# Kernel tuning notes

Measured on AMD Instinct MI355X. Metric: run time of the kernel, lower is better.

The kernel has to match this reference:

```python
import jax, jax.numpy as jnp
import numpy as np

B, S, E, H = 4, 2048, 1024, 16
HD = E // H  # 64


def setup_inputs() -> dict:
    key = jax.random.key(0)
    k1, k2, k3, k4, k5 = jax.random.split(key, 5)
    scale = 0.02
    return {
        "hidden_states": jax.random.normal(k1, (B, S, E), dtype=jnp.float32),
        "c_attn_w": jax.random.normal(k2, (E, 3 * E), dtype=jnp.float32) * scale,
        "c_attn_b": jnp.zeros((3 * E,), dtype=jnp.float32),
        "c_proj_w": jax.random.normal(k3, (E, E), dtype=jnp.float32) * scale,
        "c_proj_b": jnp.zeros((E,), dtype=jnp.float32),
    }


def reference(hidden_states, c_attn_w, c_attn_b, c_proj_w, c_proj_b):
    b, s, e = hidden_states.shape
    h, hd = H, HD
    # Conv1D: x @ W + b
    qkv = hidden_states @ c_attn_w + c_attn_b                     # [B,S,3E]
    # Faithful to source: split heads BEFORE splitting q/k/v
    qkv = qkv.reshape(b, s, h, 3 * hd).transpose(0, 2, 1, 3)      # [B,H,S,3*hd]
    q, k, v = jnp.split(qkv, 3, axis=-1)                          # each [B,H,S,hd]
    scores = jnp.einsum("bhqd,bhkd->bhqk", q, k) / (hd ** 0.5)    # [B,H,S,S]
    causal = jnp.tril(jnp.ones((s, s), dtype=bool))
    masked_bias = jnp.asarray(-10000.0, dtype=scores.dtype)
    scores = jnp.where(causal, scores, masked_bias)
    attn_weights = jax.nn.softmax(scores, axis=-1)                # [B,H,S,S]
    attn_out = jnp.einsum("bhqk,bhkd->bhqd", attn_weights, v)     # [B,H,S,hd]
    attn_out = attn_out.transpose(0, 2, 1, 3).reshape(b, s, e)    # merge heads
    out = attn_out @ c_proj_w + c_proj_b                          # [B,S,E]
    return out
```

## Files before the change

### kernel.cpp

```cpp
#include <hip/hip_runtime.h>

typedef __attribute__((ext_vector_type(8))) __bf16 bf16x8;
typedef __attribute__((ext_vector_type(2))) __bf16 bf16x2;
typedef __attribute__((ext_vector_type(8))) unsigned short u16x8;
typedef __attribute__((ext_vector_type(4))) float f32x4;
typedef __attribute__((ext_vector_type(16))) float f32x16;
typedef __attribute__((ext_vector_type(2))) unsigned int u32x2;
typedef __attribute__((ext_vector_type(4))) unsigned int u32x4;
typedef unsigned short u16;
typedef unsigned int u32;

constexpr int Bb = 4, Ss = 2048, Ee = 1024, Hh = 16, HDd = 64;
constexpr int Mm = Bb * Ss;
constexpr int N3 = 3 * Ee;
constexpr float QSC = 0.18033688011112042f;
constexpr int BHSTRIDE = Ss * HDd;
constexpr float M0 = 8.0f;

__device__ __forceinline__ u16 f2bf(float f) {
  u32 u = __builtin_bit_cast(u32, f);
  u = (u + 0x7FFFu + ((u >> 16) & 1u)) >> 16;
  return (u16)u;
}
__device__ __forceinline__ u32 pk2(float a, float b) {
  bf16x2 t;
  t[0] = (__bf16)a;
  t[1] = (__bf16)b;
  return __builtin_bit_cast(u32, t);
}
__device__ __forceinline__ float ex2(float x) {
#if __has_builtin(__builtin_amdgcn_exp2f)
  return __builtin_amdgcn_exp2f(x);
#else
  float r;
  asm volatile("v_exp_f32 %0, %1" : "=v"(r) : "v"(x));
  return r;
#endif
}

__device__ __forceinline__ void gload_lds16(const void* g, void* l) {
  __builtin_amdgcn_global_load_lds(
      (__attribute__((address_space(1))) void*)g,
      (__attribute__((address_space(3))) void*)l, 16, 0, 0);
}

__device__ __forceinline__ f32x4 mfma16(bf16x8 a, bf16x8 b, f32x4 c) {
  return __builtin_amdgcn_mfma_f32_16x16x32_bf16(a, b, c, 0, 0, 0);
}
__device__ __forceinline__ f32x16 mfma32(bf16x8 a, bf16x8 b, f32x16 c) {
  return __builtin_amdgcn_mfma_f32_32x32x16_bf16(a, b, c, 0, 0, 0);
}

__global__ void cast_x_kernel(const float* __restrict__ x, u16* __restrict__ xb, int n4) {
  int i = blockIdx.x * blockDim.x + threadIdx.x;
  int stride = gridDim.x * blockDim.x;
  for (; i < n4; i += stride) {
    float4 v = reinterpret_cast<const float4*>(x)[i];
    ushort4 o;
    o.x = f2bf(v.x); o.y = f2bf(v.y); o.z = f2bf(v.z); o.w = f2bf(v.w);
    reinterpret_cast<ushort4*>(xb)[i] = o;
  }
}

__global__ void transpose_cast_kernel(const float* __restrict__ W, u16* __restrict__ Wt,
                                      int K, int N) {
  __shared__ float tile[32][33];
  int n0 = blockIdx.x * 32, k0 = blockIdx.y * 32;
  int tx = threadIdx.x & 31, ty = threadIdx.x >> 5;
#pragma unroll
  for (int i = 0; i < 4; ++i)
    tile[ty + i * 8][tx] = W[(size_t)(k0 + ty + i * 8) * N + n0 + tx];
  __syncthreads();
#pragma unroll
  for (int i = 0; i < 4; ++i)
    Wt[(size_t)(n0 + ty + i * 8) * K + k0 + tx] = f2bf(tile[tx][ty + i * 8]);
}

template <int MODE>
__global__ __launch_bounds__(512, 1) void gemm_pipe(
    const u16* __restrict__ A, const u16* __restrict__ Bt,
    const float* __restrict__ bias, int xtiles, int cpx,
    float* __restrict__ Cout, u16* __restrict__ Qr,
    u16* __restrict__ Kp, u16* __restrict__ Vp) {
  extern __shared__ __attribute__((aligned(16))) u16 dyn[];
  constexpr int K = 1024, NT = 16;
  constexpr int BUFSTRIDE = 24576;

  int f = blockIdx.x;
  int swz = (f & 7) * cpx + (f >> 3);
  int bx = swz % xtiles, by = swz / xtiles;
  int m0 = by * 128, n0 = bx * 256;

  int tid = threadIdx.x, lane = tid & 63, wid = tid >> 6;
  int wr = wid >> 2, wc = wid & 3;
  int l7 = lane & 7, l8 = lane >> 3;
  int swcol = (l7 ^ l8) * 8;

  const u16* Ab = A + (size_t)(m0 + l8) * K + swcol;
  const u16* Bb = Bt + (size_t)(n0 + l8) * K + swcol;

  f32x4 acc[4][4];
  const f32x4 fz = {0.f, 0.f, 0.f, 0.f};
#pragma unroll
  for (int mi = 0; mi < 4; ++mi)
#pragma unroll
    for (int nj = 0; nj < 4; ++nj) acc[mi][nj] = fz;

  auto STA = [&](int tt, int c) {
    int ch = wid * 2 + c;
    gload_lds16(Ab + (size_t)(ch * 8) * K + tt * 64,
                dyn + (tt % 3) * BUFSTRIDE + ch * 512);
  };
  auto STB = [&](int tt, int c) {
    int ch = wid * 4 + c;
    gload_lds16(Bb + (size_t)(ch * 8) * K + tt * 64,
                dyn + (tt % 3) * BUFSTRIDE + 8192 + ch * 512);
  };
  auto LDA = [&](const u16* buf, int mi, int ks) -> bf16x8 {
    int row = wr * 64 + mi * 16 + (lane & 15);
    int j = ((ks * 4 + (lane >> 4)) ^ l7) * 8;
    return *(const bf16x8*)&buf[row * 64 + j];
  };
  auto LDB = [&](const u16* buf, int ni, int ks) -> bf16x8 {
    int row = wc * 64 + ni * 16 + (lane & 15);
    int j = ((ks * 4 + (lane >> 4)) ^ l7) * 8;
    return *(const bf16x8*)&buf[row * 64 + j];
  };

#pragma unroll
  for (int c = 0; c < 2; ++c) STA(0, c);
#pragma unroll
  for (int c = 0; c < 4; ++c) STB(0, c);
#pragma unroll
  for (int c = 0; c < 2; ++c) STA(1, c);
#pragma unroll
  for (int c = 0; c < 4; ++c) STB(1, c);

  for (int t = 0; t < NT; ++t) {
    const u16* Ar = dyn + (t % 3) * BUFSTRIDE;
    const u16* Br = Ar + 8192;
    if (t + 1 < NT)
      asm volatile("s_waitcnt vmcnt(6)" ::: "memory");
    else
      asm volatile("s_waitcnt vmcnt(0)" ::: "memory");
    __builtin_amdgcn_sched_barrier(0);
    __builtin_amdgcn_s_barrier();
    __builtin_amdgcn_sched_barrier(0);

    bool pre2 = (t + 2) < NT;
#pragma unroll
    for (int kk = 0; kk < 2; ++kk) {
      bf16x8 af[4], bfr[4];
#pragma unroll
      for (int mi = 0; mi < 4; ++mi) af[mi] = LDA(Ar, mi, kk);
#pragma unroll
      for (int ni = 0; ni < 4; ++ni) bfr[ni] = LDB(Br, ni, kk);
      if (kk == 0 && pre2) { STA(t + 2, 0); STA(t + 2, 1); }
      if (kk == 1 && pre2) { STB(t + 2, 0); STB(t + 2, 1); STB(t + 2, 2); STB(t + 2, 3); }
      __builtin_amdgcn_s_setprio(1);
#pragma unroll
      for (int mi = 0; mi < 4; ++mi)
#pragma unroll
        for (int ni = 0; ni < 4; ++ni)
          acc[mi][ni] = mfma16(af[mi], bfr[ni], acc[mi][ni]);
      __builtin_amdgcn_s_setprio(0);
      asm volatile("" ::: "memory");
    }
  }
  __syncthreads();

  if (MODE == 0) {
    int Nn = xtiles * 256;
#pragma unroll
    for (int nj = 0; nj < 4; ++nj) {
      int n = n0 + wc * 64 + nj * 16 + (lane & 15);
      float bn = bias[n];
#pragma unroll
      for (int mi = 0; mi < 4; ++mi)
#pragma unroll
        for (int r = 0; r < 4; ++r) {
          int m = m0 + wr * 64 + mi * 16 + (lane >> 4) * 4 + r;
          Cout[(size_t)m * Nn + n] = acc[mi][nj][r] + bn;
        }
    }
  } else {
    int gi0 = bx * 4;
    int bb = m0 >> 11;
    int mrow0 = m0 & 2047;
#pragma unroll
    for (int p = 0; p < 2; ++p) {
      if ((wc >> 1) == p) {
        int gg = wc & 1;
        int gi = gi0 + p * 2 + gg;
        int typ = gi % 3;
        float cs = (typ == 0) ? QSC : 1.0f;
#pragma unroll
        for (int nj = 0; nj < 4; ++nj) {
          int dl = nj * 16 + (lane & 15);
          float bn = bias[gi * 64 + dl];
#pragma unroll
          for (int mi = 0; mi < 4; ++mi)
#pragma unroll
            for (int r = 0; r < 4; ++r) {
              int row = wr * 64 + mi * 16 + (lane >> 4) * 4 + r;
              dyn[(gg * 128 + row) * 72 + dl] = f2bf((acc[mi][nj][r] + bn) * cs);
            }
        }
      }
      __syncthreads();
#pragma unroll
      for (int gg = 0; gg < 2; ++gg) {
        int gi = gi0 + p * 2 + gg;
        int typ = gi % 3, h = gi / 3;
        size_t basebh = (size_t)(bb * 16 + h) * BHSTRIDE;
        if (typ == 2) {
#pragma unroll
          for (int i = 0; i < 2; ++i) {
            int c = tid + 512 * i;
            int dl = c & 63, s64 = (c >> 6) & 1, kv8 = c >> 7;
            u16x8 val;
            int lrow = gg * 128 + s64 * 64 + kv8 * 8;
#pragma unroll
            for (int e = 0; e < 8; ++e) val[e] = dyn[(lrow + e) * 72 + dl];
            int tile = (mrow0 >> 6) + s64;
            size_t o = basebh + (size_t)tile * 4096 + (dl >> 5) * 2048 +
                       (kv8 >> 1) * 512 + (kv8 & 1) * 256 + (dl & 31) * 8;
            *(u16x8*)(Vp + o) = val;
          }
        } else {
#pragma unroll
          for (int i = 0; i < 2; ++i) {
            int c = tid + 512 * i;
            int sl = c >> 3, dc = c & 7;
            u16x8 val = *(const u16x8*)&dyn[(gg * 128 + sl) * 72 + dc * 8];
            int srw = mrow0 + sl;
            if (typ == 0) {
              *(u16x8*)(Qr + basebh + (size_t)srw * 64 + dc * 8) = val;
            } else {
              int tile = srw >> 6, rl = srw & 63;
              size_t o = basebh + (size_t)tile * 4096 + (rl >> 5) * 2048 +
                         (dc >> 1) * 512 + (dc & 1) * 256 + (rl & 31) * 8;
              *(u16x8*)(Kp + o) = val;
            }
          }
        }
      }
      __syncthreads();
    }
  }
}

__global__ __launch_bounds__(256) void attn_kernel(const u16* __restrict__ Qr,
                                                   const u16* __restrict__ Kp,
                                                   const u16* __restrict__ Vp,
                                                   u16* __restrict__ aout) {
  __shared__ float mbuf[2][64][33];

  int bh = blockIdx.x;
  int j = gridDim.y - 1 - blockIdx.y;
  int tid = threadIdx.x, w = tid >> 6, lane = tid & 63;
  int hi = lane >> 5, ln31 = lane & 31;
  int qrow = 32 * j + ln31;
  int nt = (j >> 1) + 1;
  int par = (j & 1) ? 32 : 0;

  size_t basebh = (size_t)bh * BHSTRIDE;
  const u16* kpb = Kp + basebh + hi * 256 + ln31 * 8;
  const u16* vpb = Vp + basebh + hi * 256 + ln31 * 8;

  bf16x8 qf[4];
#pragma unroll
  for (int kc = 0; kc < 4; ++kc)
    qf[kc] = *(const bf16x8*)(Qr + basebh + (size_t)qrow * 64 + kc * 16 + hi * 8);

  f32x16 o[2];
#pragma unroll
  for (int dm = 0; dm < 2; ++dm)
#pragma unroll
    for (int e = 0; e < 16; ++e) o[dm][e] = 0.f;
  float lrun = 0.f;

  for (int t = w; t < nt; t += 4) {
    const u16* kpt = kpb + (size_t)t * 4096;
    const u16* vpt = vpb + (size_t)t * 4096;
    bf16x8 kf[2][4], vf[2][4];
#pragma unroll
    for (int mt = 0; mt < 2; ++mt)
#pragma unroll
      for (int kc = 0; kc < 4; ++kc)
        kf[mt][kc] = *(const bf16x8*)(kpt + mt * 2048 + kc * 512);
#pragma unroll
    for (int dm = 0; dm < 2; ++dm)
#pragma unroll
      for (int kw = 0; kw < 4; ++kw)
        vf[dm][kw] = *(const bf16x8*)(vpt + dm * 2048 + kw * 512);

    f32x16 sc[2];
#pragma unroll
    for (int mt = 0; mt < 2; ++mt)
#pragma unroll
      for (int e = 0; e < 16; ++e) sc[mt][e] = -M0;
    __builtin_amdgcn_s_setprio(1);
#pragma unroll
    for (int mt = 0; mt < 2; ++mt)
#pragma unroll
      for (int kc = 0; kc < 4; ++kc)
        sc[mt] = mfma32(kf[mt][kc], qf[kc], sc[mt]);
    __builtin_amdgcn_s_setprio(0);

    if (t == nt - 1) {
#pragma unroll
      for (int mt = 0; mt < 2; ++mt)
#pragma unroll
        for (int r = 0; r < 16; ++r) {
          bool msk = (32 * mt + (r & 3) + 8 * (r >> 2) + 4 * hi) > (ln31 + par);
          sc[mt][r] = msk ? -__builtin_inff() : sc[mt][r];
        }
    }
    float s0a = 0.f, s1a = 0.f, s2a = 0.f, s3a = 0.f;
#pragma unroll
    for (int mt = 0; mt < 2; ++mt)
#pragma unroll
      for (int r = 0; r < 16; ++r) {
        float e = ex2(sc[mt][r]);
        sc[mt][r] = e;
        if ((r & 3) == 0) s0a += e;
        else if ((r & 3) == 1) s1a += e;
        else if ((r & 3) == 2) s2a += e;
        else s3a += e;
      }
    float sum = (s0a + s1a) + (s2a + s3a);
    sum += __shfl_xor(sum, 32);
    lrun += sum;

#pragma unroll
    for (int kw = 0; kw < 4; ++kw) {
      int mt = kw >> 1, k8 = (kw & 1) * 8;
      u32 a0 = pk2(sc[mt][k8 + 0], sc[mt][k8 + 1]);
      u32 a1 = pk2(sc[mt][k8 + 2], sc[mt][k8 + 3]);
      u32 b0 = pk2(sc[mt][k8 + 4], sc[mt][k8 + 5]);
      u32 b1 = pk2(sc[mt][k8 + 6], sc[mt][k8 + 7]);
      u32x2 r0 = __builtin_amdgcn_permlane32_swap(a0, b0, false, false);
      u32x2 r1 = __builtin_amdgcn_permlane32_swap(a1, b1, false, false);
      u32x4 fw;
      fw.x = r0.x;
      fw.y = r1.x;
      fw.z = r0.y;
      fw.w = r1.y;
      bf16x8 pf = __builtin_bit_cast(bf16x8, fw);
      __builtin_amdgcn_s_setprio(1);
#pragma unroll
      for (int dm = 0; dm < 2; ++dm)
        o[dm] = mfma32(vf[dm][kw], pf, o[dm]);
      __builtin_amdgcn_s_setprio(0);
    }
  }

  if (w >= 2) {
    mbuf[w - 2][lane][0] = lrun;
#pragma unroll
    for (int dm = 0; dm < 2; ++dm)
#pragma unroll
      for (int e = 0; e < 16; ++e) mbuf[w - 2][lane][1 + dm * 16 + e] = o[dm][e];
  }
  __syncthreads();
  if (w < 2) {
    lrun += mbuf[w][lane][0];
#pragma unroll
    for (int dm = 0; dm < 2; ++dm)
#pragma unroll
      for (int e = 0; e < 16; ++e) o[dm][e] += mbuf[w][lane][1 + dm * 16 + e];
  }
  __syncthreads();
  if (w == 1) {
    mbuf[0][lane][0] = lrun;
#pragma unroll
    for (int dm = 0; dm < 2; ++dm)
#pragma unroll
      for (int e = 0; e < 16; ++e) mbuf[0][lane][1 + dm * 16 + e] = o[dm][e];
  }
  __syncthreads();
  if (w == 0) {
    lrun += mbuf[0][lane][0];
#pragma unroll
    for (int dm = 0; dm < 2; ++dm)
#pragma unroll
      for (int e = 0; e < 16; ++e) o[dm][e] += mbuf[0][lane][1 + dm * 16 + e];
    int b = bh >> 4, h = bh & 15;
    float inv = 1.f / lrun;
    u16* orow = aout + (size_t)(b * Ss + qrow) * Ee + h * HDd;
#pragma unroll
    for (int dm = 0; dm < 2; ++dm)
#pragma unroll
      for (int g = 0; g < 4; ++g) {
        ushort4 st;
        st.x = f2bf(o[dm][4 * g + 0] * inv);
        st.y = f2bf(o[dm][4 * g + 1] * inv);
        st.z = f2bf(o[dm][4 * g + 2] * inv);
        st.w = f2bf(o[dm][4 * g + 3] * inv);
        *(ushort4*)(orow + 32 * dm + 8 * g + 4 * hi) = st;
      }
  }
}

extern "C" void kernel_launch(void* const* d_in, const int* in_sizes, int n_in,
                              void* d_out, int out_size, void* d_ws, size_t ws_size,
                              hipStream_t stream) {
  const float* hs        = (const float*)d_in[0];
  const float* c_attn_w  = (const float*)d_in[1];
  const float* c_attn_b  = (const float*)d_in[2];
  const float* c_proj_w  = (const float*)d_in[3];
  const float* c_proj_b  = (const float*)d_in[4];
  float* out = (float*)d_out;

  char* ws = (char*)d_ws;
  size_t off = 0;
  u16* xb     = (u16*)(ws + off); off += (size_t)Mm * Ee * 2;
  u16* wqkvt  = (u16*)(ws + off); off += (size_t)N3 * Ee * 2;
  u16* wprojt = (u16*)(ws + off); off += (size_t)Ee * Ee * 2;
  u16* Qr     = (u16*)(ws + off); off += (size_t)64 * BHSTRIDE * 2;
  u16* Kp     = (u16*)(ws + off); off += (size_t)64 * BHSTRIDE * 2;
  u16* Vp     = (u16*)(ws + off); off += (size_t)64 * BHSTRIDE * 2;
  u16* aoutb  = (u16*)(ws + off); off += (size_t)Mm * Ee * 2;
  if (ws_size < off) return;

  (void)hipFuncSetAttribute(reinterpret_cast<const void*>(gemm_pipe<1>),
                            hipFuncAttributeMaxDynamicSharedMemorySize, 147456);
  (void)hipFuncSetAttribute(reinterpret_cast<const void*>(gemm_pipe<0>),
                            hipFuncAttributeMaxDynamicSharedMemorySize, 147456);

  cast_x_kernel<<<2048, 256, 0, stream>>>(hs, xb, Mm * Ee / 4);
  transpose_cast_kernel<<<dim3(N3 / 32, Ee / 32), 256, 0, stream>>>(c_attn_w, wqkvt, Ee, N3);
  transpose_cast_kernel<<<dim3(Ee / 32, Ee / 32), 256, 0, stream>>>(c_proj_w, wprojt, Ee, Ee);
  gemm_pipe<1><<<768, 512, 147456, stream>>>(
      xb, wqkvt, c_attn_b, 12, 96, nullptr, Qr, Kp, Vp);
  attn_kernel<<<dim3(Bb * Hh, 64), 256, 0, stream>>>(Qr, Kp, Vp, aoutb);
  gemm_pipe<0><<<256, 512, 147456, stream>>>(
      aoutb, wprojt, c_proj_b, 4, 32, out, nullptr, nullptr, nullptr);
}
```

Before: 156.5 us.

## Use 256x256 tiles for the QKV GEMM with a dedicated double-buffered kernel

Adds a separate QKV projection kernel that computes 256x256 output tiles per workgroup (each wave holds 128x64) instead of 128x256. This halves the grid to 384 blocks and raises arithmetic intensity per LDS load. The pipeline drops from three stages to two, with a full vmcnt(0) wait and barrier every k-step. The epilogue scatter into Q/K/V is widened to 256 rows. Risks are fewer blocks than a multiple of the CU count (tail imbalance), higher register pressure from 32 accumulators, and less latency hiding from the shallower pipeline.

```diff
diff --git a/kernel.cpp b/kernel.cpp
--- a/kernel.cpp
+++ b/kernel.cpp
@@ -76,12 +76,160 @@
     Wt[(size_t)(n0 + ty + i * 8) * K + k0 + tx] = f2bf(tile[tx][ty + i * 8]);
 }
 
-template <int MODE>
-__global__ __launch_bounds__(512, 1) void gemm_pipe(
+__global__ __launch_bounds__(512, 1) void gemm256_qkv(
+    const u16* __restrict__ A, const u16* __restrict__ Bt,
+    const float* __restrict__ bias,
+    u16* __restrict__ Qr, u16* __restrict__ Kp, u16* __restrict__ Vp) {
+  extern __shared__ __attribute__((aligned(16))) u16 dyn[];
+  constexpr int K = 1024, NT = 16;
+
+  int f = blockIdx.x;
+  int swz = (f & 7) * 48 + (f >> 3);
+  int bx = swz % 12, by = swz / 12;
+  int m0 = by * 256, n0 = bx * 256;
+
+  int tid = threadIdx.x, lane = tid & 63, wid = tid >> 6;
+  int wr = wid >> 2, wc = wid & 3;
+  int l7 = lane & 7, l8 = lane >> 3;
+  int swcol = (l7 ^ l8) * 8;
+
+  const u16* Ab = A + (size_t)(m0 + l8) * K + swcol;
+  const u16* Bb = Bt + (size_t)(n0 + l8) * K + swcol;
+
+  f32x4 acc[8][4];
+  const f32x4 fz = {0.f, 0.f, 0.f, 0.f};
+#pragma unroll
+  for (int mi = 0; mi < 8; ++mi)
+#pragma unroll
+    for (int nj = 0; nj < 4; ++nj) acc[mi][nj] = fz;
+
+  auto STA = [&](int tt, int c) {
+    int ch = wid * 4 + c;
+    gload_lds16(Ab + (size_t)(ch * 8) * K + tt * 64,
+                dyn + (tt & 1) * 16384 + ch * 512);
+  };
+  auto STB = [&](int tt, int c) {
+    int ch = wid * 4 + c;
+    gload_lds16(Bb + (size_t)(ch * 8) * K + tt * 64,
+                dyn + 32768 + (tt & 1) * 16384 + ch * 512);
+  };
+  auto LDA = [&](const u16* buf, int mi, int ks) -> bf16x8 {
+    int row = wr * 128 + mi * 16 + (lane & 15);
+    int j = ((ks * 4 + (lane >> 4)) ^ l7) * 8;
+    return *(const bf16x8*)&buf[row * 64 + j];
+  };
+  auto LDB = [&](const u16* buf, int ni, int ks) -> bf16x8 {
+    int row = wc * 64 + ni * 16 + (lane & 15);
+    int j = ((ks * 4 + (lane >> 4)) ^ l7) * 8;
+    return *(const bf16x8*)&buf[row * 64 + j];
+  };
+
+#pragma unroll
+  for (int c = 0; c < 4; ++c) STA(0, c);
+#pragma unroll
+  for (int c = 0; c < 4; ++c) STB(0, c);
+
+  for (int t = 0; t < NT; ++t) {
+    const u16* Ar = dyn + (t & 1) * 16384;
+    const u16* Br = dyn + 32768 + (t & 1) * 16384;
+    asm volatile("s_waitcnt vmcnt(0)" ::: "memory");
+    __builtin_amdgcn_sched_barrier(0);
+    __builtin_amdgcn_s_barrier();
+    __builtin_amdgcn_sched_barrier(0);
+    if (t + 1 < NT) {
+#pragma unroll
+      for (int c = 0; c < 4; ++c) STA(t + 1, c);
+#pragma unroll
+      for (int c = 0; c < 4; ++c) STB(t + 1, c);
+    }
+#pragma unroll
+    for (int kk = 0; kk < 2; ++kk) {
+      bf16x8 bfr[4];
+#pragma unroll
+      for (int ni = 0; ni < 4; ++ni) bfr[ni] = LDB(Br, ni, kk);
+#pragma unroll
+      for (int mi = 0; mi < 8; ++mi) {
+        bf16x8 af = LDA(Ar, mi, kk);
+        __builtin_amdgcn_s_setprio(1);
+#pragma unroll
+        for (int ni = 0; ni < 4; ++ni)
+          acc[mi][ni] = mfma16(af, bfr[ni], acc[mi][ni]);
+        __builtin_amdgcn_s_setprio(0);
+      }
+      asm volatile("" ::: "memory");
+    }
+  }
+  __syncthreads();
+
+  int gi0 = bx * 4;
+  int bb = m0 >> 11;
+  int mrow0 = m0 & 2047;
+#pragma unroll
+  for (int p = 0; p < 2; ++p) {
+    if ((wc >> 1) == p) {
+      int gg = wc & 1;
+      int gi = gi0 + p * 2 + gg;
+      int typ = gi % 3;
+      float cs = (typ == 0) ? QSC : 1.0f;
+#pragma unroll
+      for (int nj = 0; nj < 4; ++nj) {
+        int dl = nj * 16 + (lane & 15);
+        float bn = bias[gi * 64 + dl];
+#pragma unroll
+        for (int mi = 0; mi < 8; ++mi)
+#pragma unroll
+          for (int r = 0; r < 4; ++r) {
+            int row = wr * 128 + mi * 16 + (lane >> 4) * 4 + r;
+            dyn[(gg * 256 + row) * 72 + dl] = f2bf((acc[mi][nj][r] + bn) * cs);
+          }
+      }
+    }
+    __syncthreads();
+#pragma unroll
+    for (int gg = 0; gg < 2; ++gg) {
+      int gi = gi0 + p * 2 + gg;
+      int typ = gi % 3, h = gi / 3;
+      size_t basebh = (size_t)(bb * 16 + h) * BHSTRIDE;
+      if (typ == 2) {
+#pragma unroll
+        for (int i = 0; i < 4; ++i) {
+          int c = tid + 512 * i;
+          int dl = c & 63, tsel = (c >> 6) & 3, kv8 = c >> 8;
+          u16x8 val;
+          int lrow = gg * 256 + tsel * 64 + kv8 * 8;
+#pragma unroll
+          for (int e = 0; e < 8; ++e) val[e] = dyn[(lrow + e) * 72 + dl];
+          int tile = (mrow0 >> 6) + tsel;
+          size_t o = basebh + (size_t)tile * 4096 + (dl >> 5) * 2048 +
+                     (kv8 >> 1) * 512 + (kv8 & 1) * 256 + (dl & 31) * 8;
+          *(u16x8*)(Vp + o) = val;
+        }
+      } else {
+#pragma unroll
+        for (int i = 0; i < 4; ++i) {
+          int c = tid + 512 * i;
+          int sl = c >> 3, dc = c & 7;
+          u16x8 val = *(const u16x8*)&dyn[(gg * 256 + sl) * 72 + dc * 8];
+          int srw = mrow0 + sl;
+          if (typ == 0) {
+            *(u16x8*)(Qr + basebh + (size_t)srw * 64 + dc * 8) = val;
+          } else {
+            int tile = srw >> 6, rl = srw & 63;
+            size_t o = basebh + (size_t)tile * 4096 + (rl >> 5) * 2048 +
+                       (dc >> 1) * 512 + (dc & 1) * 256 + (rl & 31) * 8;
+            *(u16x8*)(Kp + o) = val;
+          }
+        }
+      }
+    }
+    __syncthreads();
+  }
+}
+
+__global__ __launch_bounds__(512, 1) void gemm_proj(
     const u16* __restrict__ A, const u16* __restrict__ Bt,
     const float* __restrict__ bias, int xtiles, int cpx,
-    float* __restrict__ Cout, u16* __restrict__ Qr,
-    u16* __restrict__ Kp, u16* __restrict__ Vp) {
+    float* __restrict__ Cout) {
   extern __shared__ __attribute__((aligned(16))) u16 dyn[];
   constexpr int K = 1024, NT = 16;
   constexpr int BUFSTRIDE = 24576;
@@ -169,84 +317,18 @@
   }
   __syncthreads();
 
-  if (MODE == 0) {
-    int Nn = xtiles * 256;
-#pragma unroll
-    for (int nj = 0; nj < 4; ++nj) {
-      int n = n0 + wc * 64 + nj * 16 + (lane & 15);
-      float bn = bias[n];
-#pragma unroll
-      for (int mi = 0; mi < 4; ++mi)
-#pragma unroll
-        for (int r = 0; r < 4; ++r) {
-          int m = m0 + wr * 64 + mi * 16 + (lane >> 4) * 4 + r;
-          Cout[(size_t)m * Nn + n] = acc[mi][nj][r] + bn;
-        }
-    }
-  } else {
-    int gi0 = bx * 4;
-    int bb = m0 >> 11;
-    int mrow0 = m0 & 2047;
-#pragma unroll
-    for (int p = 0; p < 2; ++p) {
-      if ((wc >> 1) == p) {
-        int gg = wc & 1;
-        int gi = gi0 + p * 2 + gg;
-        int typ = gi % 3;
-        float cs = (typ == 0) ? QSC : 1.0f;
-#pragma unroll
-        for (int nj = 0; nj < 4; ++nj) {
-          int dl = nj * 16 + (lane & 15);
-          float bn = bias[gi * 64 + dl];
-#pragma unroll
-          for (int mi = 0; mi < 4; ++mi)
-#pragma unroll
-            for (int r = 0; r < 4; ++r) {
-              int row = wr * 64 + mi * 16 + (lane >> 4) * 4 + r;
-              dyn[(gg * 128 + row) * 72 + dl] = f2bf((acc[mi][nj][r] + bn) * cs);
-            }
-        }
+  int Nn = xtiles * 256;
+#pragma unroll
+  for (int nj = 0; nj < 4; ++nj) {
+    int n = n0 + wc * 64 + nj * 16 + (lane & 15);
+    float bn = bias[n];
+#pragma unroll
+    for (int mi = 0; mi < 4; ++mi)
+#pragma unroll
+      for (int r = 0; r < 4; ++r) {
+        int m = m0 + wr * 64 + mi * 16 + (lane >> 4) * 4 + r;
+        Cout[(size_t)m * Nn + n] = acc[mi][nj][r] + bn;
       }
-      __syncthreads();
-#pragma unroll
-      for (int gg = 0; gg < 2; ++gg) {
-        int gi = gi0 + p * 2 + gg;
-        int typ = gi % 3, h = gi / 3;
-        size_t basebh = (size_t)(bb * 16 + h) * BHSTRIDE;
-        if (typ == 2) {
-#pragma unroll
-          for (int i = 0; i < 2; ++i) {
-            int c = tid + 512 * i;
-            int dl = c & 63, s64 = (c >> 6) & 1, kv8 = c >> 7;
-            u16x8 val;
-            int lrow = gg * 128 + s64 * 64 + kv8 * 8;
-#pragma unroll
-            for (int e = 0; e < 8; ++e) val[e] = dyn[(lrow + e) * 72 + dl];
-            int tile = (mrow0 >> 6) + s64;
-            size_t o = basebh + (size_t)tile * 4096 + (dl >> 5) * 2048 +
-                       (kv8 >> 1) * 512 + (kv8 & 1) * 256 + (dl & 31) * 8;
-            *(u16x8*)(Vp + o) = val;
-          }
-        } else {
-#pragma unroll
-          for (int i = 0; i < 2; ++i) {
-            int c = tid + 512 * i;
-            int sl = c >> 3, dc = c & 7;
-            u16x8 val = *(const u16x8*)&dyn[(gg * 128 + sl) * 72 + dc * 8];
-            int srw = mrow0 + sl;
-            if (typ == 0) {
-              *(u16x8*)(Qr + basebh + (size_t)srw * 64 + dc * 8) = val;
-            } else {
-              int tile = srw >> 6, rl = srw & 63;
-              size_t o = basebh + (size_t)tile * 4096 + (rl >> 5) * 2048 +
-                         (dc >> 1) * 512 + (dc & 1) * 256 + (rl & 31) * 8;
-              *(u16x8*)(Kp + o) = val;
-            }
-          }
-        }
-      }
-      __syncthreads();
-    }
   }
 }
 
@@ -424,17 +506,16 @@
   u16* aoutb  = (u16*)(ws + off); off += (size_t)Mm * Ee * 2;
   if (ws_size < off) return;
 
-  (void)hipFuncSetAttribute(reinterpret_cast<const void*>(gemm_pipe<1>),
-                            hipFuncAttributeMaxDynamicSharedMemorySize, 147456);
-  (void)hipFuncSetAttribute(reinterpret_cast<const void*>(gemm_pipe<0>),
+  (void)hipFuncSetAttribute(reinterpret_cast<const void*>(gemm256_qkv),
+                            hipFuncAttributeMaxDynamicSharedMemorySize, 131072);
+  (void)hipFuncSetAttribute(reinterpret_cast<const void*>(gemm_proj),
                             hipFuncAttributeMaxDynamicSharedMemorySize, 147456);
 
   cast_x_kernel<<<2048, 256, 0, stream>>>(hs, xb, Mm * Ee / 4);
   transpose_cast_kernel<<<dim3(N3 / 32, Ee / 32), 256, 0, stream>>>(c_attn_w, wqkvt, Ee, N3);
   transpose_cast_kernel<<<dim3(Ee / 32, Ee / 32), 256, 0, stream>>>(c_proj_w, wprojt, Ee, Ee);
-  gemm_pipe<1><<<768, 512, 147456, stream>>>(
-      xb, wqkvt, c_attn_b, 12, 96, nullptr, Qr, Kp, Vp);
+  gemm256_qkv<<<384, 512, 131072, stream>>>(xb, wqkvt, c_attn_b, Qr, Kp, Vp);
   attn_kernel<<<dim3(Bb * Hh, 64), 256, 0, stream>>>(Qr, Kp, Vp, aoutb);
-  gemm_pipe<0><<<256, 512, 147456, stream>>>(
-      aoutb, wprojt, c_proj_b, 4, 32, out, nullptr, nullptr, nullptr);
-}
+  gemm_proj<<<256, 512, 147456, stream>>>(
+      aoutb, wprojt, c_proj_b, 4, 32, out);
+}
```

After: 170.0 us. 1.09x slower.
